# Performance work log

Measured on AMD Instinct MI355X. Metric: run time of the kernel, lower is better.

The kernel has to match this reference:

```python
import jax, jax.numpy as jnp
import numpy as np
from jax import lax

N_CLASS, SOS, EOS, NEG = 5, 0, 4, -10000.0


def _lstm_dir(x, Wih, Whh, bih, bhh, reverse):
    # x: (T, B, Din); PyTorch gate order i, f, g, o
    T, B, _ = x.shape
    Hd = Whh.shape[1]
    h0 = jnp.zeros((B, Hd), x.dtype)

    def step(carry, xt):
        h, c = carry
        g = xt @ Wih.T + h @ Whh.T + bih + bhh
        i, f, gg, o = jnp.split(g, 4, axis=-1)
        c = jax.nn.sigmoid(f) * c + jax.nn.sigmoid(i) * jnp.tanh(gg)
        h = jax.nn.sigmoid(o) * jnp.tanh(c)
        return (h, c), h

    xs = x[::-1] if reverse else x
    _, hs = lax.scan(step, (h0, h0), xs)
    return hs[::-1] if reverse else hs


def _forward(input_ids, tags, mask, emb, convs, lstm_params, lin_w, lin_b, transition):
    T, B = mask.shape
    x = emb[input_ids][:, None]  # (N, 1, L, E)
    pooled = []
    for w, b in convs:  # w: (K, 1, size, E)
        c = lax.conv_general_dilated(x, w, (1, 1), 'VALID',
                                     dimension_numbers=('NCHW', 'OIHW', 'NCHW'))
        c = jax.nn.relu(c[..., 0] + b[None, :, None])  # (N, K, L-size+1)
        pooled.append(jnp.max(c, axis=2))              # max-pool over length
    para = jnp.concatenate(pooled, axis=1)             # (N, 3K)
    h = para.reshape(B, T, -1).transpose(1, 0, 2)      # (T, B, 3K); equal para_len
    for (Wf, Uf, bf, cf, Wb, Ub, bb, cb) in lstm_params:  # 2-layer BiLSTM (eval: no dropout)
        hf = _lstm_dir(h, Wf, Uf, bf, cf, False)
        hb = _lstm_dir(h, Wb, Ub, bb, cb, True)
        h = jnp.concatenate([hf, hb], axis=-1)
    m = mask[..., None]
    feats = ((h * m) @ lin_w.T + lin_b) * m            # (T, B, 5)

    # CRF forward algorithm (log partition)
    alpha0 = jnp.full((B, N_CLASS), NEG, feats.dtype).at[:, SOS].set(0.0)

    def step(alpha, inp):
        feat, mt = inp
        s = alpha[:, None, :] + transition[None] + feat[:, :, None]
        new = jax.nn.logsumexp(s, axis=-1)
        return new * mt[:, None] + alpha * (1.0 - mt[:, None]), None

    alpha, _ = lax.scan(step, alpha0, (feats, mask))
    fwd_score = jax.nn.logsumexp(alpha + transition[EOS][None], axis=-1)

    # gold path score
    tags_ext = jnp.concatenate([jnp.full((1, B), SOS, tags.dtype), tags], 0)  # (T+1, B)
    emit = jnp.take_along_axis(feats, tags[..., None], axis=-1)[..., 0]       # (T, B)
    trans = transition[tags_ext[1:], tags_ext[:-1]]                           # (T, B)
    gold = jnp.sum((emit + trans) * mask, axis=0)
    lengths = mask.sum(0).astype(jnp.int32)
    last = tags_ext[lengths, jnp.arange(B)]
    gold = gold + transition[EOS, last]
    return (fwd_score - gold).sum()


def setup_inputs() -> dict:
    key = jax.random.key(0)
    ks = jax.random.split(key, 32)
    B, T, L, V, E, K, H = 8, 64, 64, 50000, 768, 256, 64
    N = B * T
    inp = {}
    inp['input_ids'] = jax.random.randint(ks[0], (N, L), 1, V)
    inp['tags'] = jax.random.randint(ks[1], (T, B), 1, 4)  # B/I/O tags
    inp['mask'] = jnp.ones((T, B), jnp.float32)
    inp['para_len'] = jnp.full((B,), T, jnp.int32)
    inp['emb'] = jax.random.normal(ks[2], (V, E)) * 0.1
    for i, sz in enumerate((3, 4, 5)):
        inp[f'cw{sz}'] = jax.random.normal(ks[3 + i], (K, 1, sz, E)) * (1.0 / np.sqrt(sz * E))
        inp[f'cb{sz}'] = jnp.zeros((K,), jnp.float32)
    kidx = 6
    for layer, din in ((0, 3 * K), (1, 2 * H)):
        for d in 'fb':
            inp[f'Wih{layer}{d}'] = jax.random.normal(ks[kidx], (4 * H, din)) * (1.0 / np.sqrt(din)); kidx += 1
            inp[f'Whh{layer}{d}'] = jax.random.normal(ks[kidx], (4 * H, H)) * (1.0 / np.sqrt(H)); kidx += 1
            inp[f'bih{layer}{d}'] = jnp.zeros((4 * H,), jnp.float32)
            inp[f'bhh{layer}{d}'] = jnp.zeros((4 * H,), jnp.float32)
    inp['lin_w'] = jax.random.normal(ks[kidx], (N_CLASS, 2 * H)) * 0.1; kidx += 1
    inp['lin_b'] = jnp.zeros((N_CLASS,), jnp.float32)
    tr = jax.random.normal(ks[kidx], (N_CLASS, N_CLASS))
    inp['transition'] = tr.at[SOS, :].set(NEG).at[:, EOS].set(NEG)
    return inp


def reference(input_ids, tags, mask, para_len, emb, cw3, cb3, cw4, cb4, cw5, cb5,
              Wih0f, Whh0f, bih0f, bhh0f, Wih0b, Whh0b, bih0b, bhh0b,
              Wih1f, Whh1f, bih1f, bhh1f, Wih1b, Whh1b, bih1b, bhh1b,
              lin_w, lin_b, transition):
    convs = ((cw3, cb3), (cw4, cb4), (cw5, cb5))
    lstm_params = ((Wih0f, Whh0f, bih0f, bhh0f, Wih0b, Whh0b, bih0b, bhh0b),
                   (Wih1f, Whh1f, bih1f, bhh1f, Wih1b, Whh1b, bih1b, bhh1b))
    return _forward(input_ids, tags, mask, emb, convs, lstm_params, lin_w, lin_b, transition)
```

## Files before the change

kernel.cpp:

```cpp
#include <hip/hip_runtime.h>
#include <cstdint>
#include <cstddef>

#define DEV __device__ __forceinline__

typedef __bf16 bf16x8 __attribute__((ext_vector_type(8)));
typedef float f32x4 __attribute__((ext_vector_type(4)));

#define NEG_VAL -10000.0f

DEV unsigned int f2bf(float f) {
    unsigned int u = __float_as_uint(f);
    return (u + 0x7FFFu + ((u >> 16) & 1u)) >> 16;
}
DEV unsigned int pk2(float a, float b) { return f2bf(a) | (f2bf(b) << 16); }

DEV float sigf(float x)  { return __builtin_amdgcn_rcpf(1.f + __expf(-x)); }
DEV float tanhff(float x){ return 2.f * __builtin_amdgcn_rcpf(1.f + __expf(-2.f * x)) - 1.f; }

__global__ void cast_all_kernel(const float* __restrict__ cw3,
                                const float* __restrict__ cw4,
                                const float* __restrict__ cw5,
                                const float* __restrict__ Wih0f,
                                const float* __restrict__ Wih0b,
                                const float* __restrict__ Wih1f,
                                const float* __restrict__ Wih1b,
                                unsigned short* __restrict__ wbc,
                                unsigned short* __restrict__ wih0c,
                                unsigned short* __restrict__ wih1c) {
    int tid = blockIdx.x * blockDim.x + threadIdx.x;
    const float* src;
    uint4* dstp;
    if (tid < 294912) {
        int g   = tid & 3;
        int col = (tid >> 2) & 255;
        int c   = (tid >> 10) % 24;
        int p   = tid / (24 * 256 * 4);
        int sz, j; const float* W;
        if (p < 3)      { sz = 3; j = p;     W = cw3; }
        else if (p < 7) { sz = 4; j = p - 3; W = cw4; }
        else            { sz = 5; j = p - 7; W = cw5; }
        src = W + ((size_t)col * sz + j) * 768 + c * 32 + g * 8;
        dstp = reinterpret_cast<uint4*>(wbc) +
               ((size_t)(p * 24 + c) * 1024 + (col >> 4) * 64 + g * 16 + (col & 15));
    } else if (tid < 294912 + 49152) {
        int u   = tid - 294912;
        int g   = u & 3;
        int col = (u >> 2) & 255;
        int kc  = (u >> 10) % 24;
        int dir = u / (24 * 256 * 4);
        const float* W = dir ? Wih0b : Wih0f;
        src = W + (size_t)col * 768 + kc * 32 + g * 8;
        dstp = reinterpret_cast<uint4*>(wih0c) +
               ((size_t)(dir * 24 + kc) * 1024 + (col >> 4) * 64 + g * 16 + (col & 15));
    } else if (tid < 294912 + 49152 + 8192) {
        int u   = tid - 294912 - 49152;
        int g   = u & 3;
        int col = (u >> 2) & 255;
        int kc  = (u >> 10) % 4;
        int dir = u / (4 * 256 * 4);
        const float* W = dir ? Wih1b : Wih1f;
        src = W + (size_t)col * 128 + kc * 32 + g * 8;
        dstp = reinterpret_cast<uint4*>(wih1c) +
               ((size_t)(dir * 4 + kc) * 1024 + (col >> 4) * 64 + g * 16 + (col & 15));
    } else return;
    float4 a = *(const float4*)(src);
    float4 b = *(const float4*)(src + 4);
    *dstp = make_uint4(pk2(a.x, a.y), pk2(a.z, a.w), pk2(b.x, b.y), pk2(b.z, b.w));
}

template<int SZ>
DEV void conv_body(const int* __restrict__ ids,
                   const float* __restrict__ emb,
                   const unsigned short* __restrict__ wbc,
                   const float* __restrict__ cb,
                   unsigned short* __restrict__ para_bf,
                   int pair, int szi, int pbase,
                   unsigned short* Xlds)
{
    int tid  = threadIdx.x;
    int lane = tid & 63;
    int wid  = tid >> 6;
    int mw   = wid >> 1;
    int nw   = wid & 1;
    int l15  = lane & 15;
    int q    = lane >> 4;
    int n0   = pair * 2;

    int srow  = tid >> 1;
    int shalf = tid & 1;
    int sid   = ids[(n0 + (srow >> 6)) * 64 + (srow & 63)];
    const float* embrow = emb + (size_t)sid * 768 + shalf * 16;
    int skey = (srow >> 1) & 3;
    int xo0 = srow * 32 + (((2 * shalf)     ^ skey) * 8);
    int xo1 = srow * 32 + (((2 * shalf + 1) ^ skey) * 8);

    int vXa[SZ][4];
    #pragma unroll
    for (int j = 0; j < SZ; j++)
        #pragma unroll
        for (int a = 0; a < 4; a++) {
            int pj = 16 * a + l15 + j; if (pj > 63) pj = 63;
            int xr = 64 * mw + pj;
            vXa[j][a] = xr * 32 + ((q ^ ((xr >> 1) & 3)) * 8);
        }
    int vlaneB = nw * 4096 + lane * 8;

    f32x4 acc[4][8];
    #pragma unroll
    for (int a = 0; a < 4; a++)
        #pragma unroll
        for (int t = 0; t < 8; t++) acc[a][t] = (f32x4){0.f, 0.f, 0.f, 0.f};

    bf16x8 bfr[2][8];
    float4 e0, e1, e2, e3;

    {
        e0 = ((const float4*)embrow)[0];
        e1 = ((const float4*)embrow)[1];
        e2 = ((const float4*)embrow)[2];
        e3 = ((const float4*)embrow)[3];
        const unsigned short* bt = wbc + (size_t)(pbase * 24) * 8192 + vlaneB;
        #pragma unroll
        for (int t = 0; t < 8; t++)
            bfr[0][t] = *(const bf16x8*)(bt + t * 512);
        uint4 p0 = make_uint4(pk2(e0.x, e0.y), pk2(e0.z, e0.w),
                              pk2(e1.x, e1.y), pk2(e1.z, e1.w));
        uint4 p1 = make_uint4(pk2(e2.x, e2.y), pk2(e2.z, e2.w),
                              pk2(e3.x, e3.y), pk2(e3.z, e3.w));
        *(uint4*)&Xlds[xo0] = p0;
        *(uint4*)&Xlds[xo1] = p1;
        asm volatile("s_waitcnt lgkmcnt(0)" ::: "memory");
        __builtin_amdgcn_s_barrier();
    }

    int cbase = pbase * 24;
    for (int c2 = 0; c2 < 24; c2 += 2, cbase += 2) {
        #pragma unroll
        for (int s2 = 0; s2 < 2 * SZ; ++s2) {
            const int half = (s2 < SZ) ? 0 : 1;
            const int j    = s2 - half * SZ;
            const int par  = s2 & 1;
            {
                const int sP = s2 + 1;
                const int offP = (sP < SZ) ? sP * 24
                               : (sP < 2 * SZ ? (sP - SZ) * 24 + 1 : 2);
                const unsigned short* bt =
                    wbc + (size_t)(cbase + offP) * 8192 + vlaneB;
                #pragma unroll
                for (int t = 0; t < 8; t++)
                    bfr[par ^ 1][t] = *(const bf16x8*)(bt + t * 512);
            }
            if (s2 == 0 || s2 == SZ) {
                int cE = half ? c2 + 2 : c2 + 1; if (cE > 23) cE = 0;
                const float* sp = embrow + cE * 32;
                e0 = ((const float4*)sp)[0];
                e1 = ((const float4*)sp)[1];
                e2 = ((const float4*)sp)[2];
                e3 = ((const float4*)sp)[3];
            }

            const unsigned short* Xb = Xlds + half * 4096;
            bf16x8 af[4];
            #pragma unroll
            for (int a = 0; a < 4; a++)
                af[a] = *(const bf16x8*)(&Xb[vXa[j][a]]);

            __builtin_amdgcn_s_setprio(1);
            #pragma unroll
            for (int a = 0; a < 4; a++)
                #pragma unroll
                for (int t = 0; t < 8; t++)
                    acc[a][t] = __builtin_amdgcn_mfma_f32_16x16x32_bf16(
                        af[a], bfr[par][t], acc[a][t], 0, 0, 0);
            __builtin_amdgcn_s_setprio(0);

            if (j == SZ - 1) {
                unsigned short* Xw = Xlds + (half ^ 1) * 4096;
                uint4 p0 = make_uint4(pk2(e0.x, e0.y), pk2(e0.z, e0.w),
                                      pk2(e1.x, e1.y), pk2(e1.z, e1.w));
                uint4 p1 = make_uint4(pk2(e2.x, e2.y), pk2(e2.z, e2.w),
                                      pk2(e3.x, e3.y), pk2(e3.z, e3.w));
                *(uint4*)&Xw[xo0] = p0;
                *(uint4*)&Xw[xo1] = p1;
                asm volatile("s_waitcnt lgkmcnt(0)" ::: "memory");
                __builtin_amdgcn_s_barrier();
            }
        }
    }

    int n = n0 + mw;
    int row = (n & 63) * 8 + (n >> 6);
    int pmax = 64 - SZ;
    #pragma unroll
    for (int t = 0; t < 8; t++) {
        int colb = 128 * nw + 16 * t;
        float bias = cb[colb + l15];
        float m = 0.0f;
        #pragma unroll
        for (int a = 0; a < 4; a++) {
            #pragma unroll
            for (int r = 0; r < 4; r++) {
                int p = 16 * a + q * 4 + r;
                float v = acc[a][t][r] + bias;
                v = v > 0.f ? v : 0.f;
                if (p <= pmax) m = v > m ? v : m;
            }
        }
        m = fmaxf(m, __shfl_xor(m, 16));
        m = fmaxf(m, __shfl_xor(m, 32));
        if (lane < 16)
            para_bf[(size_t)row * 768 + szi * 256 + colb + lane] =
                (unsigned short)f2bf(m);
    }
}

__global__ __launch_bounds__(256, 2) void conv_pool_kernel(
    const int* __restrict__ ids,
    const float* __restrict__ emb,
    const unsigned short* __restrict__ wbc,
    const float* __restrict__ cb3, const float* __restrict__ cb4,
    const float* __restrict__ cb5,
    unsigned short* __restrict__ para_bf)
{
    __shared__ unsigned short Xlds[2][4096];
    int bx   = blockIdx.x;
    int szi  = bx >> 8;
    int pair = bx & 255;
    if (szi == 0)
        conv_body<3>(ids, emb, wbc, cb3, para_bf, pair, 0, 0, &Xlds[0][0]);
    else if (szi == 1)
        conv_body<4>(ids, emb, wbc, cb4, para_bf, pair, 1, 3, &Xlds[0][0]);
    else
        conv_body<5>(ids, emb, wbc, cb5, para_bf, pair, 2, 7, &Xlds[0][0]);
}

template<int KC>
__global__ __launch_bounds__(256) void gemm_in_kernel(
    const unsigned short* __restrict__ xbf,
    const unsigned short* __restrict__ wihc,
    const float* __restrict__ bihF, const float* __restrict__ bhhF,
    const float* __restrict__ bihB, const float* __restrict__ bhhB,
    float* __restrict__ gates)
{
    const int din = KC * 32;
    int bx   = blockIdx.x;
    int dir  = bx >> 3;
    int rowg = (bx >> 1) & 3;
    int colg = bx & 1;
    int tid  = threadIdx.x;
    int lane = tid & 63;
    int wid  = tid >> 6;
    int mw   = wid >> 1;
    int nw   = wid & 1;
    int l15  = lane & 15;
    int q    = lane >> 4;

    const float* bih = dir ? bihB : bihF;
    const float* bhh = dir ? bhhB : bhhF;
    const unsigned short* wt = wihc + (size_t)dir * KC * 8192;

    const unsigned short* arow[4];
    #pragma unroll
    for (int a = 0; a < 4; a++)
        arow[a] = xbf + (size_t)(rowg * 128 + mw * 64 + a * 16 + l15) * din + q * 8;
    const unsigned short* bbase = wt + (colg * 8 + nw * 4) * 512 + lane * 8;

    f32x4 acc[4][4];
    #pragma unroll
    for (int a = 0; a < 4; a++)
        #pragma unroll
        for (int t = 0; t < 4; t++) acc[a][t] = (f32x4){0.f, 0.f, 0.f, 0.f};

    bf16x8 afb[2][4], bfb[2][4];
    #pragma unroll
    for (int a = 0; a < 4; a++) afb[0][a] = *(const bf16x8*)(arow[a]);
    #pragma unroll
    for (int t = 0; t < 4; t++) bfb[0][t] = *(const bf16x8*)(bbase + t * 512);

    #pragma unroll 2
    for (int kc = 0; kc < KC; ++kc) {
        const int p = kc & 1;
        int kn = (kc + 1 < KC) ? kc + 1 : kc;
        #pragma unroll
        for (int a = 0; a < 4; a++)
            afb[p ^ 1][a] = *(const bf16x8*)(arow[a] + kn * 32);
        #pragma unroll
        for (int t = 0; t < 4; t++)
            bfb[p ^ 1][t] = *(const bf16x8*)(bbase + (size_t)kn * 8192 + t * 512);
        __builtin_amdgcn_s_setprio(1);
        #pragma unroll
        for (int a = 0; a < 4; a++)
            #pragma unroll
            for (int t = 0; t < 4; t++)
                acc[a][t] = __builtin_amdgcn_mfma_f32_16x16x32_bf16(
                    afb[p][a], bfb[p][t], acc[a][t], 0, 0, 0);
        __builtin_amdgcn_s_setprio(0);
    }

    #pragma unroll
    for (int t = 0; t < 4; t++) {
        int nn = colg * 128 + nw * 64 + t * 16 + l15;
        float bb = bih[nn] + bhh[nn];
        float* gp = gates + ((size_t)dir * 256 + nn) * 512 +
                    rowg * 128 + mw * 64 + q * 4;
        #pragma unroll
        for (int a = 0; a < 4; a++) {
            f32x4 v = acc[a][t];
            v[0] += bb; v[1] += bb; v[2] += bb; v[3] += bb;
            *(f32x4*)(gp + a * 16) = v;
        }
    }
}

__global__ __launch_bounds__(256) void lstm_rec_kernel(
    const float* __restrict__ gates,
    const float* __restrict__ WhhF, const float* __restrict__ WhhB,
    float* __restrict__ houtF,
    unsigned short* __restrict__ houtB)
{
    int dir = blockIdx.x;
    const float* Whh = dir ? WhhB : WhhF;
    const float* gin = gates + (size_t)dir * 256 * 512;

    __shared__ unsigned short h16[2][16 * 64];

    int tid  = threadIdx.x;
    int lane = tid & 63;
    int w    = tid >> 6;
    int l15  = lane & 15;
    int q    = lane >> 4;
    int hh   = 16 * w + l15;

    bf16x8 Bf[4][2];
    #pragma unroll
    for (int g = 0; g < 4; g++)
        #pragma unroll
        for (int kh = 0; kh < 2; kh++) {
            const float* wp = Whh + (size_t)(g * 64 + hh) * 64 + kh * 32 + q * 8;
            float4 f0 = *(const float4*)wp;
            float4 f1 = *(const float4*)(wp + 4);
            bf16x8 r;
            r[0] = (__bf16)f0.x; r[1] = (__bf16)f0.y;
            r[2] = (__bf16)f0.z; r[3] = (__bf16)f0.w;
            r[4] = (__bf16)f1.x; r[5] = (__bf16)f1.y;
            r[6] = (__bf16)f1.z; r[7] = (__bf16)f1.w;
            Bf[g][kh] = r;
        }

    const float* pg0 = gin + ((size_t)(0 * 64 + hh)) * 512 + 4 * (q & 1);
    const float* pg1 = gin + ((size_t)(1 * 64 + hh)) * 512 + 4 * (q & 1);
    const float* pg2 = gin + ((size_t)(2 * 64 + hh)) * 512 + 4 * (q & 1);
    const float* pg3 = gin + ((size_t)(3 * 64 + hh)) * 512 + 4 * (q & 1);

    for (int i = tid; i < 2 * 16 * 64; i += 256)
        ((unsigned short*)h16)[i] = 0;
    float cst[4] = {0.f, 0.f, 0.f, 0.f};
    __syncthreads();

    int t0 = dir ? 63 : 0;
    f32x4 gv0 = *(const f32x4*)(pg0 + t0 * 8);
    f32x4 gv1 = *(const f32x4*)(pg1 + t0 * 8);
    f32x4 gv2 = *(const f32x4*)(pg2 + t0 * 8);
    f32x4 gv3 = *(const f32x4*)(pg3 + t0 * 8);

    for (int s = 0; s < 64; ++s) {
        int t = dir ? 63 - s : s;
        const unsigned short* hb = h16[s & 1];
        int slot0 = q ^ (l15 & 7);
        int slot1 = (4 + q) ^ (l15 & 7);
        bf16x8 a0 = *(const bf16x8*)&hb[l15 * 64 + slot0 * 8];
        bf16x8 a1 = *(const bf16x8*)&hb[l15 * 64 + slot1 * 8];

        f32x4 zero = (f32x4){0.f, 0.f, 0.f, 0.f};
        f32x4 acc[4];
        #pragma unroll
        for (int g = 0; g < 4; g++) {
            acc[g] = __builtin_amdgcn_mfma_f32_16x16x32_bf16(a0, Bf[g][0], zero, 0, 0, 0);
            acc[g] = __builtin_amdgcn_mfma_f32_16x16x32_bf16(a1, Bf[g][1], acc[g], 0, 0, 0);
        }

        int sn = (s + 1 < 64) ? s + 1 : 63;
        int t2 = dir ? 63 - sn : sn;
        f32x4 n0 = *(const f32x4*)(pg0 + t2 * 8);
        f32x4 n1 = *(const f32x4*)(pg1 + t2 * 8);
        f32x4 n2 = *(const f32x4*)(pg2 + t2 * 8);
        f32x4 n3 = *(const f32x4*)(pg3 + t2 * 8);

        if (q < 2) {
            unsigned short* hw = h16[(s + 1) & 1];
            #pragma unroll
            for (int r = 0; r < 4; r++) {
                int b = 4 * q + r;
                float gi = acc[0][r] + gv0[r];
                float gf = acc[1][r] + gv1[r];
                float gg = acc[2][r] + gv2[r];
                float go = acc[3][r] + gv3[r];
                float cn = sigf(gf) * cst[r] + sigf(gi) * tanhff(gg);
                float hv = sigf(go) * tanhff(cn);
                cst[r] = cn;
                int slot = (hh >> 3) ^ (b & 7);
                hw[b * 64 + slot * 8 + (hh & 7)] = (unsigned short)f2bf(hv);
                size_t oi = ((size_t)t * 8 + b) * 128 + dir * 64 + hh;
                houtF[oi] = hv;
                houtB[oi] = (unsigned short)f2bf(hv);
            }
        }
        __syncthreads();
        gv0 = n0; gv1 = n1; gv2 = n2; gv3 = n3;
    }
}

__global__ __launch_bounds__(512) void crf_kernel(
    const float* __restrict__ h1,
    const float* __restrict__ lin_w,
    const float* __restrict__ lin_b,
    const float* __restrict__ mask,
    const int* __restrict__ tags,
    const float* __restrict__ trans,
    float* __restrict__ out) {
    __shared__ float feats[64][8][5];
    __shared__ float wl[5][128];
    __shared__ float msk[512];
    __shared__ int   tgs[512];
    __shared__ float fwd_s[8], gold_s[8];
    __shared__ float tr[25], trE[5], lb[5];
    int tid = threadIdx.x;
    if (tid < 25) tr[tid] = trans[tid];
    if (tid < 5) { trE[tid] = trans[20 + tid]; lb[tid] = lin_b[tid]; }
    msk[tid] = mask[tid];
    tgs[tid] = tags[tid];
    if (tid < 128) {
        #pragma unroll
        for (int i = 0; i < 5; i++) wl[i][tid] = lin_w[i * 128 + tid];
    }
    __syncthreads();

    {
        const float4* h4 = (const float4*)(h1 + (size_t)tid * 128);
        float a0 = 0.f, a1 = 0.f, a2 = 0.f, a3 = 0.f, a4 = 0.f;
        for (int e4 = 0; e4 < 32; e4++) {
            float4 hv = h4[e4];
            int e = e4 * 4;
            a0 += hv.x * wl[0][e] + hv.y * wl[0][e+1] + hv.z * wl[0][e+2] + hv.w * wl[0][e+3];
            a1 += hv.x * wl[1][e] + hv.y * wl[1][e+1] + hv.z * wl[1][e+2] + hv.w * wl[1][e+3];
            a2 += hv.x * wl[2][e] + hv.y * wl[2][e+1] + hv.z * wl[2][e+2] + hv.w * wl[2][e+3];
            a3 += hv.x * wl[3][e] + hv.y * wl[3][e+1] + hv.z * wl[3][e+2] + hv.w * wl[3][e+3];
            a4 += hv.x * wl[4][e] + hv.y * wl[4][e+1] + hv.z * wl[4][e+2] + hv.w * wl[4][e+3];
        }
        float m = msk[tid];
        int t = tid >> 3, b = tid & 7;
        feats[t][b][0] = (m * a0 + lb[0]) * m;
        feats[t][b][1] = (m * a1 + lb[1]) * m;
        feats[t][b][2] = (m * a2 + lb[2]) * m;
        feats[t][b][3] = (m * a3 + lb[3]) * m;
        feats[t][b][4] = (m * a4 + lb[4]) * m;
    }
    __syncthreads();

    if (tid < 40) {
        int b = tid / 5, i = tid % 5;
        float alpha = (i == 0) ? 0.f : NEG_VAL;
        float trow[5];
        #pragma unroll
        for (int j2 = 0; j2 < 5; j2++) trow[j2] = tr[i * 5 + j2];
        for (int t = 0; t < 64; t++) {
            float s0, s1, s2, s3, s4;
            s0 = __shfl(alpha, b * 5 + 0, 64) + trow[0];
            s1 = __shfl(alpha, b * 5 + 1, 64) + trow[1];
            s2 = __shfl(alpha, b * 5 + 2, 64) + trow[2];
            s3 = __shfl(alpha, b * 5 + 3, 64) + trow[3];
            s4 = __shfl(alpha, b * 5 + 4, 64) + trow[4];
            float mx = fmaxf(fmaxf(fmaxf(s0, s1), fmaxf(s2, s3)), s4);
            float sum = expf(s0 - mx) + expf(s1 - mx) + expf(s2 - mx) +
                        expf(s3 - mx) + expf(s4 - mx);
            float lse = mx + logf(sum) + feats[t][b][i];
            float mt = msk[t * 8 + b];
            alpha = mt * lse + (1.f - mt) * alpha;
        }
        float v = alpha + trE[i];
        float m0 = __shfl(v, b * 5 + 0, 64);
        float m1 = __shfl(v, b * 5 + 1, 64);
        float m2 = __shfl(v, b * 5 + 2, 64);
        float m3 = __shfl(v, b * 5 + 3, 64);
        float m4 = __shfl(v, b * 5 + 4, 64);
        float mx = fmaxf(fmaxf(fmaxf(m0, m1), fmaxf(m2, m3)), m4);
        float sum = expf(m0 - mx) + expf(m1 - mx) + expf(m2 - mx) +
                    expf(m3 - mx) + expf(m4 - mx);
        if (i == 0) fwd_s[b] = mx + logf(sum);
    }
    if (tid >= 64 && tid < 72) {
        int b = tid - 64;
        float g = 0.f, lenf = 0.f;
        int prev = 0;
        for (int t = 0; t < 64; t++) {
            int tg = tgs[t * 8 + b];
            float mt = msk[t * 8 + b];
            g += (feats[t][b][tg] + tr[tg * 5 + prev]) * mt;
            lenf += mt;
            prev = tg;
        }
        int len = (int)lenf;
        int last = (len == 0) ? 0 : tgs[(len - 1) * 8 + b];
        g += trE[last];
        gold_s[b] = g;
    }
    __syncthreads();
    if (tid == 0) {
        float s = 0.f;
        for (int b = 0; b < 8; b++) s += fwd_s[b] - gold_s[b];
        out[0] = s;
    }
}

extern "C" void kernel_launch(void* const* d_in, const int* in_sizes, int n_in,
                              void* d_out, int out_size, void* d_ws, size_t ws_size,
                              hipStream_t stream) {
    const int*   ids   = (const int*)d_in[0];
    const int*   tags  = (const int*)d_in[1];
    const float* mask  = (const float*)d_in[2];
    const float* emb   = (const float*)d_in[4];
    const float* cw3   = (const float*)d_in[5];
    const float* cb3   = (const float*)d_in[6];
    const float* cw4   = (const float*)d_in[7];
    const float* cb4   = (const float*)d_in[8];
    const float* cw5   = (const float*)d_in[9];
    const float* cb5   = (const float*)d_in[10];
    const float* Wih0f = (const float*)d_in[11];
    const float* Whh0f = (const float*)d_in[12];
    const float* bih0f = (const float*)d_in[13];
    const float* bhh0f = (const float*)d_in[14];
    const float* Wih0b = (const float*)d_in[15];
    const float* Whh0b = (const float*)d_in[16];
    const float* bih0b = (const float*)d_in[17];
    const float* bhh0b = (const float*)d_in[18];
    const float* Wih1f = (const float*)d_in[19];
    const float* Whh1f = (const float*)d_in[20];
    const float* bih1f = (const float*)d_in[21];
    const float* bhh1f = (const float*)d_in[22];
    const float* Wih1b = (const float*)d_in[23];
    const float* Whh1b = (const float*)d_in[24];
    const float* bih1b = (const float*)d_in[25];
    const float* bhh1b = (const float*)d_in[26];
    const float* lin_w = (const float*)d_in[27];
    const float* lin_b = (const float*)d_in[28];
    const float* trans = (const float*)d_in[29];

    char* ws = (char*)d_ws;
    unsigned short* wbc     = (unsigned short*)ws;
    unsigned short* wih0c   = (unsigned short*)(ws + 4718592);
    unsigned short* wih1c   = (unsigned short*)(ws + 5505024);
    unsigned short* para_bf = (unsigned short*)(ws + 5636096);
    float*          gates   = (float*)(ws + 6422528);
    float*          h0f     = (float*)(ws + 7471104);
    unsigned short* h0_bf   = (unsigned short*)(ws + 5636096);
    float*          h1f     = (float*)(ws + 4718592);
    unsigned short* h1_bf   = (unsigned short*)(ws + 5636096);

    hipLaunchKernelGGL(cast_all_kernel, dim3(1376), dim3(256), 0, stream,
                       cw3, cw4, cw5, Wih0f, Wih0b, Wih1f, Wih1b,
                       wbc, wih0c, wih1c);
    hipLaunchKernelGGL(conv_pool_kernel, dim3(768), dim3(256), 0, stream,
                       ids, emb, wbc, cb3, cb4, cb5, para_bf);
    hipLaunchKernelGGL((gemm_in_kernel<24>), dim3(16), dim3(256), 0, stream,
                       para_bf, wih0c, bih0f, bhh0f, bih0b, bhh0b, gates);
    hipLaunchKernelGGL(lstm_rec_kernel, dim3(2), dim3(256), 0, stream,
                       gates, Whh0f, Whh0b, h0f, h0_bf);
    hipLaunchKernelGGL((gemm_in_kernel<4>), dim3(16), dim3(256), 0, stream,
                       h0_bf, wih1c, bih1f, bhh1f, bih1b, bhh1b, gates);
    hipLaunchKernelGGL(lstm_rec_kernel, dim3(2), dim3(256), 0, stream,
                       gates, Whh1f, Whh1b, h1f, h1_bf);
    hipLaunchKernelGGL(crf_kernel, dim3(1), dim3(512), 0, stream,
                       h1f, lin_w, lin_b, mask, tags, trans, (float*)d_out);
}
```

Baseline: 287.5 us.

## Retile conv waves to cover both sequences and skip unused layer-0 float output

```diff
diff --git a/kernel.cpp b/kernel.cpp
--- a/kernel.cpp
+++ b/kernel.cpp
@@ -80,9 +80,7 @@
 {
     int tid  = threadIdx.x;
     int lane = tid & 63;
-    int wid  = tid >> 6;
-    int mw   = wid >> 1;
-    int nw   = wid & 1;
+    int nw   = tid >> 6;
     int l15  = lane & 15;
     int q    = lane >> 4;
     int n0   = pair * 2;
@@ -95,24 +93,15 @@
     int xo0 = srow * 32 + (((2 * shalf)     ^ skey) * 8);
     int xo1 = srow * 32 + (((2 * shalf + 1) ^ skey) * 8);
 
-    int vXa[SZ][4];
-    #pragma unroll
-    for (int j = 0; j < SZ; j++)
-        #pragma unroll
-        for (int a = 0; a < 4; a++) {
-            int pj = 16 * a + l15 + j; if (pj > 63) pj = 63;
-            int xr = 64 * mw + pj;
-            vXa[j][a] = xr * 32 + ((q ^ ((xr >> 1) & 3)) * 8);
-        }
-    int vlaneB = nw * 4096 + lane * 8;
-
-    f32x4 acc[4][8];
-    #pragma unroll
-    for (int a = 0; a < 4; a++)
-        #pragma unroll
-        for (int t = 0; t < 8; t++) acc[a][t] = (f32x4){0.f, 0.f, 0.f, 0.f};
-
-    bf16x8 bfr[2][8];
+    int vlaneB = nw * 2048 + lane * 8;
+
+    f32x4 acc[8][4];
+    #pragma unroll
+    for (int a = 0; a < 8; a++)
+        #pragma unroll
+        for (int t = 0; t < 4; t++) acc[a][t] = (f32x4){0.f, 0.f, 0.f, 0.f};
+
+    bf16x8 bfr[2][4];
     float4 e0, e1, e2, e3;
 
     {
@@ -122,7 +111,7 @@
         e3 = ((const float4*)embrow)[3];
         const unsigned short* bt = wbc + (size_t)(pbase * 24) * 8192 + vlaneB;
         #pragma unroll
-        for (int t = 0; t < 8; t++)
+        for (int t = 0; t < 4; t++)
             bfr[0][t] = *(const bf16x8*)(bt + t * 512);
         uint4 p0 = make_uint4(pk2(e0.x, e0.y), pk2(e0.z, e0.w),
                               pk2(e1.x, e1.y), pk2(e1.z, e1.w));
@@ -148,7 +137,7 @@
                 const unsigned short* bt =
                     wbc + (size_t)(cbase + offP) * 8192 + vlaneB;
                 #pragma unroll
-                for (int t = 0; t < 8; t++)
+                for (int t = 0; t < 4; t++)
                     bfr[par ^ 1][t] = *(const bf16x8*)(bt + t * 512);
             }
             if (s2 == 0 || s2 == SZ) {
@@ -161,19 +150,41 @@
             }
 
             const unsigned short* Xb = Xlds + half * 4096;
-            bf16x8 af[4];
-            #pragma unroll
-            for (int a = 0; a < 4; a++)
-                af[a] = *(const bf16x8*)(&Xb[vXa[j][a]]);
-
-            __builtin_amdgcn_s_setprio(1);
-            #pragma unroll
-            for (int a = 0; a < 4; a++)
+            {
+                bf16x8 af[4];
                 #pragma unroll
-                for (int t = 0; t < 8; t++)
-                    acc[a][t] = __builtin_amdgcn_mfma_f32_16x16x32_bf16(
-                        af[a], bfr[par][t], acc[a][t], 0, 0, 0);
-            __builtin_amdgcn_s_setprio(0);
+                for (int a = 0; a < 4; a++) {
+                    int pp = 16 * a + l15 + j; if (pp > 63) pp = 63;
+                    af[a] = *(const bf16x8*)(
+                        &Xb[pp * 32 + ((q ^ ((pp >> 1) & 3)) * 8)]);
+                }
+                __builtin_amdgcn_s_setprio(1);
+                #pragma unroll
+                for (int a = 0; a < 4; a++)
+                    #pragma unroll
+                    for (int t = 0; t < 4; t++)
+                        acc[a][t] = __builtin_amdgcn_mfma_f32_16x16x32_bf16(
+                            af[a], bfr[par][t], acc[a][t], 0, 0, 0);
+                __builtin_amdgcn_s_setprio(0);
+            }
+            {
+                bf16x8 af[4];
+                #pragma unroll
+                for (int a = 0; a < 4; a++) {
+                    int pp = 16 * a + l15 + j; if (pp > 63) pp = 63;
+                    int xr = 64 + pp;
+                    af[a] = *(const bf16x8*)(
+                        &Xb[xr * 32 + ((q ^ ((xr >> 1) & 3)) * 8)]);
+                }
+                __builtin_amdgcn_s_setprio(1);
+                #pragma unroll
+                for (int a = 0; a < 4; a++)
+                    #pragma unroll
+                    for (int t = 0; t < 4; t++)
+                        acc[4 + a][t] = __builtin_amdgcn_mfma_f32_16x16x32_bf16(
+                            af[a], bfr[par][t], acc[4 + a][t], 0, 0, 0);
+                __builtin_amdgcn_s_setprio(0);
+            }
 
             if (j == SZ - 1) {
                 unsigned short* Xw = Xlds + (half ^ 1) * 4096;
@@ -189,29 +200,33 @@
         }
     }
 
-    int n = n0 + mw;
-    int row = (n & 63) * 8 + (n >> 6);
     int pmax = 64 - SZ;
     #pragma unroll
-    for (int t = 0; t < 8; t++) {
-        int colb = 128 * nw + 16 * t;
+    for (int t = 0; t < 4; t++) {
+        int colb = nw * 64 + t * 16;
         float bias = cb[colb + l15];
-        float m = 0.0f;
-        #pragma unroll
-        for (int a = 0; a < 4; a++) {
+        #pragma unroll
+        for (int s = 0; s < 2; s++) {
+            float m = 0.0f;
             #pragma unroll
-            for (int r = 0; r < 4; r++) {
-                int p = 16 * a + q * 4 + r;
-                float v = acc[a][t][r] + bias;
-                v = v > 0.f ? v : 0.f;
-                if (p <= pmax) m = v > m ? v : m;
-            }
-        }
-        m = fmaxf(m, __shfl_xor(m, 16));
-        m = fmaxf(m, __shfl_xor(m, 32));
-        if (lane < 16)
-            para_bf[(size_t)row * 768 + szi * 256 + colb + lane] =
-                (unsigned short)f2bf(m);
+            for (int a4 = 0; a4 < 4; a4++) {
+                #pragma unroll
+                for (int r = 0; r < 4; r++) {
+                    int p = 16 * a4 + q * 4 + r;
+                    float v = acc[s * 4 + a4][t][r] + bias;
+                    v = v > 0.f ? v : 0.f;
+                    if (p <= pmax) m = v > m ? v : m;
+                }
+            }
+            m = fmaxf(m, __shfl_xor(m, 16));
+            m = fmaxf(m, __shfl_xor(m, 32));
+            if (lane < 16) {
+                int n = n0 + s;
+                int row = (n & 63) * 8 + (n >> 6);
+                para_bf[(size_t)row * 768 + szi * 256 + colb + lane] =
+                    (unsigned short)f2bf(m);
+            }
+        }
     }
 }
 
@@ -402,7 +417,7 @@
                 int slot = (hh >> 3) ^ (b & 7);
                 hw[b * 64 + slot * 8 + (hh & 7)] = (unsigned short)f2bf(hv);
                 size_t oi = ((size_t)t * 8 + b) * 128 + dir * 64 + hh;
-                houtF[oi] = hv;
+                if (houtF) houtF[oi] = hv;
                 houtB[oi] = (unsigned short)f2bf(hv);
             }
         }
@@ -552,10 +567,8 @@
     unsigned short* wih1c   = (unsigned short*)(ws + 5505024);
     unsigned short* para_bf = (unsigned short*)(ws + 5636096);
     float*          gates   = (float*)(ws + 6422528);
-    float*          h0f     = (float*)(ws + 7471104);
     unsigned short* h0_bf   = (unsigned short*)(ws + 5636096);
     float*          h1f     = (float*)(ws + 4718592);
-    unsigned short* h1_bf   = (unsigned short*)(ws + 5636096);
 
     hipLaunchKernelGGL(cast_all_kernel, dim3(1376), dim3(256), 0, stream,
                        cw3, cw4, cw5, Wih0f, Wih0b, Wih1f, Wih1b,
@@ -565,11 +578,11 @@
     hipLaunchKernelGGL((gemm_in_kernel<24>), dim3(16), dim3(256), 0, stream,
                        para_bf, wih0c, bih0f, bhh0f, bih0b, bhh0b, gates);
     hipLaunchKernelGGL(lstm_rec_kernel, dim3(2), dim3(256), 0, stream,
-                       gates, Whh0f, Whh0b, h0f, h0_bf);
+                       gates, Whh0f, Whh0b, (float*)nullptr, h0_bf);
     hipLaunchKernelGGL((gemm_in_kernel<4>), dim3(16), dim3(256), 0, stream,
                        h0_bf, wih1c, bih1f, bhh1f, bih1b, bhh1b, gates);
     hipLaunchKernelGGL(lstm_rec_kernel, dim3(2), dim3(256), 0, stream,
-                       gates, Whh1f, Whh1b, h1f, h1_bf);
+                       gates, Whh1f, Whh1b, h1f, h0_bf);
     hipLaunchKernelGGL(crf_kernel, dim3(1), dim3(512), 0, stream,
                        h1f, lin_w, lin_b, mask, tags, trans, (float*)d_out);
 }
```

Measured after the change: 283.0 us. Within noise of the previous version (-1.6%).
